# Performance work log

Hardware: AMD Instinct MI355X
Metric: run time of the kernel (lower is better)

## Reference

```python
import jax, jax.numpy as jnp
import numpy as np

BATCH = 32768
NUM_CLASSES = 1024  # balanced binary hierarchy => 10 levels, 1023 internal nodes


def setup_inputs() -> dict:
    key = jax.random.key(0)
    outputs = jax.random.normal(key, (BATCH, NUM_CLASSES), dtype=jnp.float32)
    return {"outputs": outputs}


def reference(outputs) -> jnp.ndarray:
    """SoftEmbeddedDecisionRules.forward for a balanced binary hierarchy.

    For every internal node: child logit = mean of raw logits over the child's
    leaf (class) set, softmax over the node's children, then multiply each
    class's running probability by the prob of the branch containing it.
    With a balanced binary tree over C classes, level l has 2^l nodes, each
    child covering a contiguous block of C / 2^(l+1) classes, so the per-node
    Python loop of the original collapses into one reshape+mean+softmax per
    level (log2(C) fused passes total).
    """
    B, C = outputs.shape
    depth = C.bit_length() - 1  # log2(C), static
    class_probs = jnp.ones((B, C), dtype=outputs.dtype)
    for level in range(depth):
        n_nodes = 1 << level
        seg = C // (2 * n_nodes)  # classes per child subtree
        # node logits: mean of raw logits over each child's class block
        node_logits = outputs.reshape(B, n_nodes, 2, seg).mean(axis=-1)  # [B, n, 2]
        probs = jax.nn.softmax(node_logits, axis=-1)  # softmax over children
        # scatter-multiply child prob onto every class in that child's subtree
        expanded = jnp.broadcast_to(probs[..., None], (B, n_nodes, 2, seg)).reshape(B, C)
        class_probs = class_probs * expanded
    return class_probs
```

## Files before the change

kernel.cpp:

```cpp
#include <hip/hip_runtime.h>


#define C 1024

__device__ __forceinline__ float sigmoid_of(float x) {
    return __builtin_amdgcn_rcpf(1.0f + __expf(x));
}

__global__ __launch_bounds__(256) void hier_softmax_kernel(
    const float* __restrict__ in, float* __restrict__ out) {
    const int tid  = threadIdx.x;
    const int lane = tid & 63;
    const int wave = tid >> 6;
    const int row  = (blockIdx.x << 2) + wave;

    const float* rowp = in + (size_t)row * C;

    float4 L[4];
    L[0] = ((const float4*)(rowp +   0))[lane];
    L[1] = ((const float4*)(rowp + 256))[lane];
    L[2] = ((const float4*)(rowp + 512))[lane];
    L[3] = ((const float4*)(rowp + 768))[lane];

    float pA[4], pB[4], p2[4], sum[4], com[4];
#pragma unroll
    for (int q = 0; q < 4; ++q) {
        const float s2a = L[q].x + L[q].y;
        const float s2b = L[q].z + L[q].w;
        pA[q]  = sigmoid_of(L[q].y - L[q].x);
        pB[q]  = sigmoid_of(L[q].w - L[q].z);
        p2[q]  = sigmoid_of((s2b - s2a) * 0.5f);
        sum[q] = s2a + s2b;
        com[q] = 1.0f;
    }

    float inv_seg = 0.25f;
#pragma unroll
    for (int k = 1; k <= 32; k <<= 1) {
        float pr[4];
#pragma unroll
        for (int q = 0; q < 4; ++q) pr[q] = __shfl_xor(sum[q], k, 64);
#pragma unroll
        for (int q = 0; q < 4; ++q) {
            com[q] *= sigmoid_of((pr[q] - sum[q]) * inv_seg);
            sum[q] += pr[q];
        }
        inv_seg *= 0.5f;
    }

    const float pRoot = sigmoid_of((sum[2] + sum[3] - sum[0] - sum[1]) * (1.0f / 512.0f));
    const float pL    = sigmoid_of((sum[1] - sum[0]) * (1.0f / 256.0f));
    const float pR    = sigmoid_of((sum[3] - sum[2]) * (1.0f / 256.0f));
    float t[4];
    t[0] = pRoot * pL;          t[1] = pRoot - t[0];
    const float rRoot = 1.0f - pRoot;
    t[2] = rRoot * pR;          t[3] = rRoot - t[2];

    float* orow = out + (size_t)row * C;
#pragma unroll
    for (int q = 0; q < 4; ++q) {
        const float base = t[q] * com[q];
        const float cl = base * p2[q];
        const float cr = base - cl;
        float4 o;
        o.x = cl * pA[q];
        o.y = cl - o.x;
        o.z = cr * pB[q];
        o.w = cr - o.z;
        ((float4*)(orow + q * 256))[lane] = o;
    }
}

extern "C" void kernel_launch(void* const* d_in, const int* in_sizes, int n_in,
                              void* d_out, int out_size, void* d_ws, size_t ws_size,
                              hipStream_t stream) {
    const float* in = (const float*)d_in[0];
    float* out = (float*)d_out;
    const int B = in_sizes[0] / C;
    hier_softmax_kernel<<<B / 4, 256, 0, stream>>>(in, out);
}
```

Before: 228.1 us.

## Process four rows per wave with double-buffered register prefetch

Each wave now handles four consecutive rows instead of one. The next row's loads are issued before the current row is processed, using two alternating register sets. The aim is to hide global memory latency behind the sigmoid and shuffle work and to spread block launch overhead over more rows. In exchange the grid is four times smaller and register pressure is higher, which can lower occupancy on a purely bandwidth-bound kernel.

```diff
diff --git a/kernel.cpp b/kernel.cpp
--- a/kernel.cpp
+++ b/kernel.cpp
@@ -2,26 +2,24 @@
 
 
 #define C 1024
+#define ROWS_PER_WAVE 4
 
 __device__ __forceinline__ float sigmoid_of(float x) {
     return __builtin_amdgcn_rcpf(1.0f + __expf(x));
 }
 
-__global__ __launch_bounds__(256) void hier_softmax_kernel(
-    const float* __restrict__ in, float* __restrict__ out) {
-    const int tid  = threadIdx.x;
-    const int lane = tid & 63;
-    const int wave = tid >> 6;
-    const int row  = (blockIdx.x << 2) + wave;
+__device__ __forceinline__ void load_row(const float* __restrict__ rowp, int lane,
+                                         float4& q0, float4& q1, float4& q2, float4& q3) {
+    q0 = ((const float4*)(rowp +   0))[lane];
+    q1 = ((const float4*)(rowp + 256))[lane];
+    q2 = ((const float4*)(rowp + 512))[lane];
+    q3 = ((const float4*)(rowp + 768))[lane];
+}
 
-    const float* rowp = in + (size_t)row * C;
-
-    float4 L[4];
-    L[0] = ((const float4*)(rowp +   0))[lane];
-    L[1] = ((const float4*)(rowp + 256))[lane];
-    L[2] = ((const float4*)(rowp + 512))[lane];
-    L[3] = ((const float4*)(rowp + 768))[lane];
-
+__device__ __forceinline__ void process_row(const float4 L0, const float4 L1,
+                                            const float4 L2, const float4 L3,
+                                            float* __restrict__ orow, int lane) {
+    const float4 L[4] = {L0, L1, L2, L3};
     float pA[4], pB[4], p2[4], sum[4], com[4];
 #pragma unroll
     for (int q = 0; q < 4; ++q) {
@@ -56,7 +54,6 @@
     const float rRoot = 1.0f - pRoot;
     t[2] = rRoot * pR;          t[3] = rRoot - t[2];
 
-    float* orow = out + (size_t)row * C;
 #pragma unroll
     for (int q = 0; q < 4; ++q) {
         const float base = t[q] * com[q];
@@ -71,11 +68,34 @@
     }
 }
 
+__global__ __launch_bounds__(256) void hier_softmax_kernel(
+    const float* __restrict__ in, float* __restrict__ out) {
+    const int lane = threadIdx.x & 63;
+    const int gw   = blockIdx.x * 4 + (threadIdx.x >> 6);
+    const size_t r0 = (size_t)gw * ROWS_PER_WAVE;
+
+    const float* ip = in  + r0 * C;
+    float*       op = out + r0 * C;
+
+    float4 a0, a1, a2, a3;
+    float4 b0, b1, b2, b3;
+
+    load_row(ip + 0 * C, lane, a0, a1, a2, a3);
+    load_row(ip + 1 * C, lane, b0, b1, b2, b3);
+    process_row(a0, a1, a2, a3, op + 0 * C, lane);
+    load_row(ip + 2 * C, lane, a0, a1, a2, a3);
+    process_row(b0, b1, b2, b3, op + 1 * C, lane);
+    load_row(ip + 3 * C, lane, b0, b1, b2, b3);
+    process_row(a0, a1, a2, a3, op + 2 * C, lane);
+    process_row(b0, b1, b2, b3, op + 3 * C, lane);
+}
+
 extern "C" void kernel_launch(void* const* d_in, const int* in_sizes, int n_in,
                               void* d_out, int out_size, void* d_ws, size_t ws_size,
                               hipStream_t stream) {
     const float* in = (const float*)d_in[0];
     float* out = (float*)d_out;
     const int B = in_sizes[0] / C;
-    hier_softmax_kernel<<<B / 4, 256, 0, stream>>>(in, out);
+    const int blocks = B / (4 * ROWS_PER_WAVE);
+    hier_softmax_kernel<<<blocks, 256, 0, stream>>>(in, out);
 }
```

Result: slower. 234.6 us (+2.8%).
